# Performance work log

Hardware: AMD Instinct MI355X
Metric: run time of the kernel (lower is better)

Reference implementation:

```python
import jax, jax.numpy as jnp
import numpy as np

DIM = 2048
N_HEAD = 16
HEAD_DIM = DIM // N_HEAD


def setup_inputs() -> dict:
    key = jax.random.key(0)
    ks = jax.random.split(key, 7)
    B, N = 2, 2048
    s = 1.0 / np.sqrt(DIM)
    return {
        "x": jax.random.normal(ks[0], (B, N, DIM), dtype=jnp.float32),
        "Wq": jax.random.normal(ks[1], (DIM, DIM), dtype=jnp.float32) * s,
        "bq": jnp.zeros((DIM,), dtype=jnp.float32),
        "Wkv": jax.random.normal(ks[2], (DIM, 2 * HEAD_DIM), dtype=jnp.float32) * s,
        "bkv": jnp.zeros((2 * HEAD_DIM,), dtype=jnp.float32),
        "Wo": jax.random.normal(ks[3], (DIM, DIM), dtype=jnp.float32) * s,
        "bo": jnp.zeros((DIM,), dtype=jnp.float32),
    }


def reference(x, Wq, bq, Wkv, bkv, Wo, bo):
    B, N, D = x.shape
    # Q projection -> (B, H, N, hd)
    q = (x @ Wq + bq).reshape(B, N, N_HEAD, HEAD_DIM).transpose(0, 2, 1, 3)
    # shared single-head K/V (kv = x, self-attention path)
    kvp = x @ Wkv + bkv  # (B, M, 2*hd)
    k, v = kvp[..., :HEAD_DIM], kvp[..., HEAD_DIM:]  # (B, M, hd) each
    scale = 1.0 / np.sqrt(HEAD_DIM).astype(np.float32)
    # broadcast shared K over heads without materializing expanded K/V
    scores = jnp.einsum("bhnd,bmd->bhnm", q, k) * scale  # (B, H, N, M)
    attn = jax.nn.softmax(scores, axis=-1)
    out = jnp.einsum("bhnm,bmd->bhnd", attn, v)  # (B, H, N, hd)
    out = out.transpose(0, 2, 1, 3).reshape(B, N, D)
    return out @ Wo + bo
```

## Files before the change

kernel.cpp:

```cpp
#include <hip/hip_runtime.h>
#include <math.h>

using bf16x8 = __attribute__((ext_vector_type(8))) short;
using f32x4  = __attribute__((ext_vector_type(4))) float;
using f32x16 = __attribute__((ext_vector_type(16))) float;
using u16x4  = __attribute__((ext_vector_type(4))) unsigned short;
using u32x4  = __attribute__((ext_vector_type(4))) unsigned int;

#define DIMSZ 2048
#define NSEQ  2048
#define BATCH 2
#define NHEAD 16
#define HD    128

__device__ __forceinline__ unsigned short f2bf(float x) {
    unsigned int u = __builtin_bit_cast(unsigned int, x);
    unsigned int r = (u + 0x7FFFu + ((u >> 16) & 1u)) >> 16;
    return (unsigned short)r;
}

__device__ __forceinline__ unsigned int cvtpk_bf16(float lo, float hi) {
    unsigned int r;
    asm("v_cvt_pk_bf16_f32 %0, %1, %2" : "=v"(r) : "v"(lo), "v"(hi));
    return r;
}

__device__ __forceinline__ void gload_lds16(const unsigned short* g, unsigned short* l) {
    __builtin_amdgcn_global_load_lds(
        (const __attribute__((address_space(1))) unsigned int*)g,
        (__attribute__((address_space(3))) unsigned int*)l, 16, 0, 0);
}

__global__ void k_cast_bf16(const float* __restrict__ in, unsigned short* __restrict__ out, int n4) {
    int i = blockIdx.x * blockDim.x + threadIdx.x;
    if (i >= n4) return;
    f32x4 v = *(const f32x4*)(in + (size_t)i * 4);
    u16x4 o;
#pragma unroll
    for (int j = 0; j < 4; j++) o[j] = f2bf(v[j]);
    *(u16x4*)(out + (size_t)i * 4) = o;
}

__global__ void k_transpose_all(const float* __restrict__ Wq, const float* __restrict__ Wkv,
                                const float* __restrict__ Wo, unsigned short* __restrict__ wqkvt,
                                unsigned short* __restrict__ wot, float sc) {
    __shared__ float t[32][33];
    const int ct = blockIdx.x;
    const int k0 = blockIdx.y * 32;
    const float* src;
    unsigned short* dst;
    float scale;
    int N, n0;
    if (ct < 64)      { src = Wq;  dst = wqkvt;                       scale = sc;   N = 2048; n0 = ct * 32; }
    else if (ct < 72) { src = Wkv; dst = wqkvt + (size_t)2048 * 2048; scale = 1.0f; N = 256;  n0 = (ct - 64) * 32; }
    else              { src = Wo;  dst = wot;                         scale = 1.0f; N = 2048; n0 = (ct - 72) * 32; }
    const int tx = threadIdx.x, ty = threadIdx.y;
#pragma unroll
    for (int i = 0; i < 32; i += 8) t[ty + i][tx] = src[(size_t)(k0 + ty + i) * N + n0 + tx];
    __syncthreads();
#pragma unroll
    for (int i = 0; i < 32; i += 8)
        dst[(size_t)(n0 + ty + i) * 2048 + k0 + tx] = f2bf(t[tx][ty + i] * scale);
}

__global__ void k_transpose_v(const unsigned short* __restrict__ kvp, unsigned short* __restrict__ vt) {
    __shared__ unsigned short t[32][33];
    int n0 = blockIdx.x * 32, d0 = blockIdx.y * 32, b = blockIdx.z;
    int tx = threadIdx.x, ty = threadIdx.y;
#pragma unroll
    for (int i = 0; i < 32; i += 8)
        t[ty + i][tx] = kvp[(size_t)(b * NSEQ + n0 + ty + i) * 256 + 128 + d0 + tx];
    __syncthreads();
#pragma unroll
    for (int i = 0; i < 32; i += 8)
        vt[(size_t)(b * HD + d0 + ty + i) * NSEQ + n0 + tx] = t[tx][ty + i];
}

__device__ __forceinline__ void xcd_tile(int nbx, int& bx, int& by) {
    int wg = ((int)blockIdx.x & 7) * ((int)gridDim.x >> 3) + ((int)blockIdx.x >> 3);
    bx = wg % nbx;
    by = wg / nbx;
}

#define GEMM_BODY(EPILOGUE)                                                                    \
    __shared__ unsigned short As[3][256 * 32];                                                 \
    __shared__ unsigned short Bs[3][128 * 32];                                                 \
    const int tid = threadIdx.x;                                                               \
    const int wid = tid >> 6;                                                                  \
    const int lane = tid & 63;                                                                 \
    const int g = lane >> 4, cc = lane & 15;                                                   \
    const int wm = wid >> 1, wn = wid & 1;                                                     \
    int bx, by;                                                                                \
    xcd_tile(nbx, bx, by);                                                                     \
    const size_t m0 = (size_t)by * 256;                                                        \
    const size_t n0 = (size_t)bx * 128;                                                        \
    f32x4 acc[4][4] = {};                                                                      \
               \
    const unsigned short* gA0 = A + (m0 + (tid >> 2)) * (size_t)K + (tid & 3) * 8;             \
    const unsigned short* gA1 = A + (m0 + 128 + (tid >> 2)) * (size_t)K + (tid & 3) * 8;       \
    const unsigned short* gB  = Bt + (n0 + (tid >> 2)) * (size_t)K + (tid & 3) * 8;            \
    const int NT = K / 32;                                                                     \
    auto STAGE = [&](int buf, int k0) {                                                        \
        gload_lds16(gA0 + k0, &As[buf][wid * 512]);                                            \
        gload_lds16(gA1 + k0, &As[buf][4096 + wid * 512]);                                     \
        gload_lds16(gB + k0, &Bs[buf][wid * 512]);                                             \
    };                                                                                         \
    STAGE(0, 0);                                                                               \
    STAGE(1, 32);                                                                              \
    for (int t = 0; t < NT; ++t) {                                                             \
        if (t < NT - 1)                                                                        \
            asm volatile("s_waitcnt vmcnt(3)" ::: "memory");                                   \
        else                                                                                   \
            asm volatile("s_waitcnt vmcnt(0)" ::: "memory");                                   \
        __builtin_amdgcn_s_barrier();                                                          \
        __builtin_amdgcn_sched_barrier(0);                                                     \
        if (t + 2 < NT) STAGE((t + 2) % 3, (t + 2) * 32);                                      \
        const unsigned short* Ac = &As[t % 3][0];                                              \
        const unsigned short* Bc = &Bs[t % 3][0];                                              \
        bf16x8 af[4], bfr[4];                                                                  \
        _Pragma("unroll") for (int mi = 0; mi < 4; mi++)                                       \
            af[mi] = *(const bf16x8*)(Ac + (wm * 64 + mi * 16 + cc) * 32 + g * 8);             \
        _Pragma("unroll") for (int ni = 0; ni < 4; ni++)                                       \
            bfr[ni] = *(const bf16x8*)(Bc + (wn * 64 + ni * 16 + cc) * 32 + g * 8);            \
        _Pragma("unroll") for (int mi = 0; mi < 4; mi++)                                       \
            _Pragma("unroll") for (int ni = 0; ni < 4; ni++)                                   \
                acc[mi][ni] = __builtin_amdgcn_mfma_f32_16x16x32_bf16(af[mi], bfr[ni],         \
                                                                      acc[mi][ni], 0, 0, 0);  \
    }                                                                                          \
    EPILOGUE

__global__ __launch_bounds__(512, 4)
void k_gemm_qkv(const unsigned short* __restrict__ A, const unsigned short* __restrict__ Bt,
                const float* __restrict__ bq, float bscale, const float* __restrict__ bkv,
                unsigned short* __restrict__ qout, unsigned short* __restrict__ kvout,
                int M, int K, int nbx) {
    GEMM_BODY({
        const bool isQ = (n0 < 2048);
        const int colg = (int)n0 + wn * 64 + cc;
        const int col0 = isQ ? colg : colg - 2048;
        const int ostride = isQ ? 2048 : 256;
        unsigned short* outp = isQ ? qout : kvout;
        float bia[4];
        _Pragma("unroll") for (int ni = 0; ni < 4; ni++)
            bia[ni] = isQ ? bq[col0 + ni * 16] * bscale : bkv[col0 + ni * 16];
        _Pragma("unroll") for (int mi = 0; mi < 4; mi++) {
            size_t row = m0 + wm * 64 + mi * 16 + g * 4;
            _Pragma("unroll") for (int ni = 0; ni < 4; ni++)
                _Pragma("unroll") for (int r = 0; r < 4; r++)
                    outp[(row + r) * ostride + col0 + ni * 16] = f2bf(acc[mi][ni][r] + bia[ni]);
        }
    })
}

__global__ __launch_bounds__(512, 4)
void k_gemm_bt_f32(const unsigned short* __restrict__ A, const unsigned short* __restrict__ Bt,
                   const float* __restrict__ bias, float* __restrict__ Cout,
                   int M, int N, int K, int nbx) {
    GEMM_BODY({
        const int col0 = (int)n0 + wn * 64 + cc;
        float bia[4];
        _Pragma("unroll") for (int ni = 0; ni < 4; ni++) bia[ni] = bias[col0 + ni * 16];
        _Pragma("unroll") for (int mi = 0; mi < 4; mi++) {
            size_t row = m0 + wm * 64 + mi * 16 + g * 4;
            _Pragma("unroll") for (int ni = 0; ni < 4; ni++)
                _Pragma("unroll") for (int r = 0; r < 4; r++)
                    Cout[(row + r) * N + col0 + ni * 16] = acc[mi][ni][r] + bia[ni];
        }
    })
}

__global__ __launch_bounds__(256, 2)
void k_attn(const unsigned short* __restrict__ q, const unsigned short* __restrict__ kvp,
            const unsigned short* __restrict__ vt, unsigned short* __restrict__ out) {
    __shared__ unsigned char Kb[2][16384];
    __shared__ unsigned char Vb[2][16384];

    const int b = blockIdx.z, h = blockIdx.y, qt = blockIdx.x;
    const int tid = threadIdx.x, w = tid >> 6, lane = tid & 63;
    const int q32 = lane & 31, hi = lane >> 5;

    const int qrow = qt * 128 + w * 32 + q32;
    const unsigned short* qp = q + (size_t)(b * NSEQ + qrow) * DIMSZ + h * HD + hi * 8;
    bf16x8 qf[8];
#pragma unroll
    for (int dc = 0; dc < 8; dc++) qf[dc] = *(const bf16x8*)(qp + dc * 16);

    const char* kvpc = (const char*)kvp;
    const char* vtc  = (const char*)vt;
    size_t srcK[4], srcV[4];
#pragma unroll
    for (int c = 0; c < 4; c++) {
        unsigned int o = (tid + c * 256) * 16;
        unsigned int krow = o >> 8, kcol = o & 255;
        srcK[c] = (size_t)(b * NSEQ + krow) * 512 + (kcol ^ (((krow >> 1) & 15) << 4));
        unsigned int vrow = o >> 7, vcol = o & 127;
        srcV[c] = (size_t)(b * HD + vrow) * 4096 + (vcol ^ (((vrow >> 2) & 7) << 4));
    }

    auto STAGE = [&](int buf, int t) {
        size_t kb_ = (size_t)t * 32768;
        size_t vb_ = (size_t)t * 128;
#pragma unroll
        for (int c = 0; c < 4; c++) {
            gload_lds16((const unsigned short*)(kvpc + srcK[c] + kb_),
                        (unsigned short*)(Kb[buf] + (w * 64 + c * 256) * 16));
            gload_lds16((const unsigned short*)(vtc + srcV[c] + vb_),
                        (unsigned short*)(Vb[buf] + (w * 64 + c * 256) * 16));
        }
    };

    f32x16 o0 = {}, o1 = {}, o2 = {}, o3 = {};
    float l_run = 0.0f;
    const unsigned int swK = ((q32 >> 1) & 15) << 4;
    const unsigned int swV = ((q32 >> 2) & 7) << 4;

#define PROC_KT(S, KTB)                                                               \
    {                                                                                 \
        float pz[16];                                                                 \
        _Pragma("unroll") for (int r = 0; r < 16; r++) {                              \
            pz[r] = __builtin_amdgcn_exp2f(S[r]);                                     \
            l_run += pz[r];                                                           \
        }                                                                             \
        _Pragma("unroll") for (int kc = 0; kc < 2; kc++) {                            \
            unsigned int own01 = cvtpk_bf16(pz[kc * 8 + 0], pz[kc * 8 + 1]);          \
            unsigned int own23 = cvtpk_bf16(pz[kc * 8 + 2], pz[kc * 8 + 3]);          \
            unsigned int own45 = cvtpk_bf16(pz[kc * 8 + 4], pz[kc * 8 + 5]);          \
            unsigned int own67 = cvtpk_bf16(pz[kc * 8 + 6], pz[kc * 8 + 7]);          \
            unsigned int send_a = hi ? own01 : own45;                                 \
            unsigned int send_b = hi ? own23 : own67;                                 \
            unsigned int got_a = (unsigned int)__shfl_xor((int)send_a, 32, 64);       \
            unsigned int got_b = (unsigned int)__shfl_xor((int)send_b, 32, 64);       \
            u32x4 awv;                                                                \
            awv[0] = hi ? got_a : own01;                                              \
            awv[1] = hi ? got_b : own23;                                              \
            awv[2] = hi ? own45 : got_a;                                              \
            awv[3] = hi ? own67 : got_b;                                              \
            bf16x8 pa = __builtin_bit_cast(bf16x8, awv);                              \
            const unsigned int kbo = (KTB) + kc * 32 + hi * 16;                       \
            bf16x8 vf0 = *(const bf16x8*)(Vc + (q32 + 0) * 128 + (kbo ^ swV));        \
            bf16x8 vf1 = *(const bf16x8*)(Vc + (q32 + 32) * 128 + (kbo ^ swV));       \
            bf16x8 vf2 = *(const bf16x8*)(Vc + (q32 + 64) * 128 + (kbo ^ swV));       \
            bf16x8 vf3 = *(const bf16x8*)(Vc + (q32 + 96) * 128 + (kbo ^ swV));       \
            __builtin_amdgcn_s_setprio(1);                                            \
            o0 = __builtin_amdgcn_mfma_f32_32x32x16_bf16(pa, vf0, o0, 0, 0, 0);       \
            o1 = __builtin_amdgcn_mfma_f32_32x32x16_bf16(pa, vf1, o1, 0, 0, 0);       \
            o2 = __builtin_amdgcn_mfma_f32_32x32x16_bf16(pa, vf2, o2, 0, 0, 0);       \
            o3 = __builtin_amdgcn_mfma_f32_32x32x16_bf16(pa, vf3, o3, 0, 0, 0);       \
            __builtin_amdgcn_s_setprio(0);                                            \
        }                                                                             \
    }

    STAGE(0, 0);
    __syncthreads();

    for (int t = 0; t < NSEQ / 64; t++) {
        const int cur = t & 1;
        if (t < NSEQ / 64 - 1) STAGE(cur ^ 1, t + 1);

        const unsigned char* Kc = Kb[cur];
        const unsigned char* Vc = Vb[cur];

        f32x16 s0 = {}, s1 = {};
#pragma unroll
        for (int dc = 0; dc < 8; dc++) {
            const unsigned int db = dc * 32 + hi * 16;
            bf16x8 kf0 = *(const bf16x8*)(Kc + q32 * 256 + (db ^ swK));
            bf16x8 kf1 = *(const bf16x8*)(Kc + (q32 + 32) * 256 + (db ^ swK));
            __builtin_amdgcn_s_setprio(1);
            s0 = __builtin_amdgcn_mfma_f32_32x32x16_bf16(kf0, qf[dc], s0, 0, 0, 0);
            s1 = __builtin_amdgcn_mfma_f32_32x32x16_bf16(kf1, qf[dc], s1, 0, 0, 0);
            __builtin_amdgcn_s_setprio(0);
        }

        PROC_KT(s0, 0)
        PROC_KT(s1, 64)

        __syncthreads();
    }
#undef PROC_KT

    l_run += __shfl_xor(l_run, 32, 64);
    float* Lp = (float*)(Kb[0] + w * 128);
    if (hi == 0) Lp[q32] = l_run;

    float rinv[16];
#pragma unroll
    for (int r = 0; r < 16; r++) {
        int qloc = (r & 3) + 8 * (r >> 2) + 4 * hi;
        rinv[r] = 1.0f / Lp[qloc];
    }

    unsigned short* op = out + (size_t)(b * NSEQ + qt * 128 + w * 32) * DIMSZ + h * HD + q32;
#pragma unroll
    for (int r = 0; r < 16; r++) {
        int qloc = (r & 3) + 8 * (r >> 2) + 4 * hi;
        op[(size_t)qloc * DIMSZ + 0]  = f2bf(o0[r] * rinv[r]);
        op[(size_t)qloc * DIMSZ + 32] = f2bf(o1[r] * rinv[r]);
        op[(size_t)qloc * DIMSZ + 64] = f2bf(o2[r] * rinv[r]);
        op[(size_t)qloc * DIMSZ + 96] = f2bf(o3[r] * rinv[r]);
    }
}

extern "C" void kernel_launch(void* const* d_in, const int* in_sizes, int n_in,
                              void* d_out, int out_size, void* d_ws, size_t ws_size,
                              hipStream_t stream) {
    const float* x   = (const float*)d_in[0];
    const float* Wq  = (const float*)d_in[1];
    const float* bq  = (const float*)d_in[2];
    const float* Wkv = (const float*)d_in[3];
    const float* bkv = (const float*)d_in[4];
    const float* Wo  = (const float*)d_in[5];
    const float* bo  = (const float*)d_in[6];

    char* w = (char*)d_ws;
    unsigned short* xb    = (unsigned short*)(w);
    unsigned short* wqkvt = (unsigned short*)(w + 16777216);
    unsigned short* wot   = (unsigned short*)(w + 26214400);
    unsigned short* qb    = (unsigned short*)(w + 34603008);
    unsigned short* kvpb  = (unsigned short*)(w + 51380224);
    unsigned short* vtb   = (unsigned short*)(w + 53477376);
    unsigned short* aob   = xb;

    const float sc = 0.08838834764831845f * 1.4426950408889634f;

    k_cast_bf16<<<dim3((BATCH * NSEQ * DIMSZ / 4 + 255) / 256), dim3(256), 0, stream>>>(
        x, xb, BATCH * NSEQ * DIMSZ / 4);
    k_transpose_all<<<dim3(136, 64), dim3(32, 8), 0, stream>>>(Wq, Wkv, Wo, wqkvt, wot, sc);

    k_gemm_qkv<<<dim3((BATCH * NSEQ / 256) * (2304 / 128)), dim3(512), 0, stream>>>(
        xb, wqkvt, bq, sc, bkv, qb, kvpb, BATCH * NSEQ, DIMSZ, 2304 / 128);
    k_transpose_v<<<dim3(NSEQ / 32, HD / 32, BATCH), dim3(32, 8), 0, stream>>>(kvpb, vtb);
    k_attn<<<dim3(NSEQ / 128, NHEAD, BATCH), dim3(256), 0, stream>>>(qb, kvpb, vtb, aob);
    k_gemm_bt_f32<<<dim3((BATCH * NSEQ / 256) * (DIMSZ / 128)), dim3(512), 0, stream>>>(
        aob, wot, bo, (float*)d_out, BATCH * NSEQ, DIMSZ, DIMSZ, DIMSZ / 128);
}
```

Baseline: 224.1 us.

## Merge prep kernels, fuse V transpose into QKV GEMM, retile GEMMs

Folds the x cast and weight transpose into one launch and writes V transposed straight from the QKV GEMM epilogue, which removes two kernel launches and a separate transpose pass. The GEMMs change from 256x128 tiles with 512 threads, K-step 32 and triple buffering to 128x128 tiles with 256 threads, K-step 64 and double buffering with __syncthreads. The new GEMM gives up the fine-grained vmcnt pipelining, so loads and compute may overlap less, and the smaller tiles reuse each loaded tile less.

```diff
diff --git a/kernel.cpp b/kernel.cpp
--- a/kernel.cpp
+++ b/kernel.cpp
@@ -31,22 +31,25 @@
         (__attribute__((address_space(3))) unsigned int*)l, 16, 0, 0);
 }
 
-__global__ void k_cast_bf16(const float* __restrict__ in, unsigned short* __restrict__ out, int n4) {
-    int i = blockIdx.x * blockDim.x + threadIdx.x;
-    if (i >= n4) return;
-    f32x4 v = *(const f32x4*)(in + (size_t)i * 4);
-    u16x4 o;
-#pragma unroll
-    for (int j = 0; j < 4; j++) o[j] = f2bf(v[j]);
-    *(u16x4*)(out + (size_t)i * 4) = o;
-}
-
-__global__ void k_transpose_all(const float* __restrict__ Wq, const float* __restrict__ Wkv,
-                                const float* __restrict__ Wo, unsigned short* __restrict__ wqkvt,
-                                unsigned short* __restrict__ wot, float sc) {
+#define NCAST 8192
+__global__ void k_prep(const float* __restrict__ x, unsigned short* __restrict__ xb,
+                       const float* __restrict__ Wq, const float* __restrict__ Wkv,
+                       const float* __restrict__ Wo, unsigned short* __restrict__ wqkvt,
+                       unsigned short* __restrict__ wot, float sc) {
     __shared__ float t[32][33];
-    const int ct = blockIdx.x;
-    const int k0 = blockIdx.y * 32;
+    const int tid = threadIdx.x;
+    if ((int)blockIdx.x < NCAST) {
+        int i = blockIdx.x * 256 + tid;
+        f32x4 v = *(const f32x4*)(x + (size_t)i * 4);
+        u16x4 o;
+#pragma unroll
+        for (int j = 0; j < 4; j++) o[j] = f2bf(v[j]);
+        *(u16x4*)(xb + (size_t)i * 4) = o;
+        return;
+    }
+    const int tb = blockIdx.x - NCAST;
+    const int ct = tb % 136;
+    const int k0 = (tb / 136) * 32;
     const float* src;
     unsigned short* dst;
     float scale;
@@ -54,26 +57,13 @@
     if (ct < 64)      { src = Wq;  dst = wqkvt;                       scale = sc;   N = 2048; n0 = ct * 32; }
     else if (ct < 72) { src = Wkv; dst = wqkvt + (size_t)2048 * 2048; scale = 1.0f; N = 256;  n0 = (ct - 64) * 32; }
     else              { src = Wo;  dst = wot;                         scale = 1.0f; N = 2048; n0 = (ct - 72) * 32; }
-    const int tx = threadIdx.x, ty = threadIdx.y;
+    const int tx = tid & 31, ty = tid >> 5;
 #pragma unroll
     for (int i = 0; i < 32; i += 8) t[ty + i][tx] = src[(size_t)(k0 + ty + i) * N + n0 + tx];
     __syncthreads();
 #pragma unroll
     for (int i = 0; i < 32; i += 8)
         dst[(size_t)(n0 + ty + i) * 2048 + k0 + tx] = f2bf(t[tx][ty + i] * scale);
-}
-
-__global__ void k_transpose_v(const unsigned short* __restrict__ kvp, unsigned short* __restrict__ vt) {
-    __shared__ unsigned short t[32][33];
-    int n0 = blockIdx.x * 32, d0 = blockIdx.y * 32, b = blockIdx.z;
-    int tx = threadIdx.x, ty = threadIdx.y;
-#pragma unroll
-    for (int i = 0; i < 32; i += 8)
-        t[ty + i][tx] = kvp[(size_t)(b * NSEQ + n0 + ty + i) * 256 + 128 + d0 + tx];
-    __syncthreads();
-#pragma unroll
-    for (int i = 0; i < 32; i += 8)
-        vt[(size_t)(b * HD + d0 + ty + i) * NSEQ + n0 + tx] = t[tx][ty + i];
 }
 
 __device__ __forceinline__ void xcd_tile(int nbx, int& bx, int& by) {
@@ -82,86 +72,103 @@
     by = wg / nbx;
 }
 
-#define GEMM_BODY(EPILOGUE)                                                                    \
-    __shared__ unsigned short As[3][256 * 32];                                                 \
-    __shared__ unsigned short Bs[3][128 * 32];                                                 \
+#define GEMM_BODY64(EPILOGUE)                                                                  \
+    __shared__ unsigned short As[2][128 * 64];                                                 \
+    __shared__ unsigned short Bs[2][128 * 64];                                                 \
     const int tid = threadIdx.x;                                                               \
     const int wid = tid >> 6;                                                                  \
     const int lane = tid & 63;                                                                 \
     const int g = lane >> 4, cc = lane & 15;                                                   \
-    const int wm = wid >> 1, wn = wid & 1;                                                     \
+    const int wr = wid >> 1, wc = wid & 1;                                                     \
     int bx, by;                                                                                \
     xcd_tile(nbx, bx, by);                                                                     \
-    const size_t m0 = (size_t)by * 256;                                                        \
+    const size_t m0 = (size_t)by * 128;                                                        \
     const size_t n0 = (size_t)bx * 128;                                                        \
     f32x4 acc[4][4] = {};                                                                      \
-               \
-    const unsigned short* gA0 = A + (m0 + (tid >> 2)) * (size_t)K + (tid & 3) * 8;             \
-    const unsigned short* gA1 = A + (m0 + 128 + (tid >> 2)) * (size_t)K + (tid & 3) * 8;       \
-    const unsigned short* gB  = Bt + (n0 + (tid >> 2)) * (size_t)K + (tid & 3) * 8;            \
-    const int NT = K / 32;                                                                     \
+    const unsigned short* gA = A + (m0 + wid * 32 + (lane >> 3)) * (size_t)K + (lane & 7) * 8; \
+    const unsigned short* gB = Bt + (n0 + wid * 32 + (lane >> 3)) * (size_t)K + (lane & 7) * 8;\
     auto STAGE = [&](int buf, int k0) {                                                        \
-        gload_lds16(gA0 + k0, &As[buf][wid * 512]);                                            \
-        gload_lds16(gA1 + k0, &As[buf][4096 + wid * 512]);                                     \
-        gload_lds16(gB + k0, &Bs[buf][wid * 512]);                                             \
+        _Pragma("unroll") for (int c = 0; c < 4; c++) {                                        \
+            gload_lds16(gA + (size_t)(c * 8) * K + k0, &As[buf][(wid * 32 + c * 8) * 64]);     \
+            gload_lds16(gB + (size_t)(c * 8) * K + k0, &Bs[buf][(wid * 32 + c * 8) * 64]);     \
+        }                                                                                      \
     };                                                                                         \
     STAGE(0, 0);                                                                               \
-    STAGE(1, 32);                                                                              \
-    for (int t = 0; t < NT; ++t) {                                                             \
-        if (t < NT - 1)                                                                        \
-            asm volatile("s_waitcnt vmcnt(3)" ::: "memory");                                   \
-        else                                                                                   \
-            asm volatile("s_waitcnt vmcnt(0)" ::: "memory");                                   \
-        __builtin_amdgcn_s_barrier();                                                          \
-        __builtin_amdgcn_sched_barrier(0);                                                     \
-        if (t + 2 < NT) STAGE((t + 2) % 3, (t + 2) * 32);                                      \
-        const unsigned short* Ac = &As[t % 3][0];                                              \
-        const unsigned short* Bc = &Bs[t % 3][0];                                              \
-        bf16x8 af[4], bfr[4];                                                                  \
-        _Pragma("unroll") for (int mi = 0; mi < 4; mi++)                                       \
-            af[mi] = *(const bf16x8*)(Ac + (wm * 64 + mi * 16 + cc) * 32 + g * 8);             \
-        _Pragma("unroll") for (int ni = 0; ni < 4; ni++)                                       \
-            bfr[ni] = *(const bf16x8*)(Bc + (wn * 64 + ni * 16 + cc) * 32 + g * 8);            \
-        _Pragma("unroll") for (int mi = 0; mi < 4; mi++)                                       \
+    __syncthreads();                                                                           \
+    int cur = 0;                                                                               \
+    for (int k0 = 0; k0 < K; k0 += 64) {                                                       \
+        if (k0 + 64 < K) STAGE(cur ^ 1, k0 + 64);                                              \
+        _Pragma("unroll") for (int kk = 0; kk < 2; kk++) {                                     \
+            bf16x8 af[4], bfr[4];                                                              \
+            _Pragma("unroll") for (int mi = 0; mi < 4; mi++)                                   \
+                af[mi] = *(const bf16x8*)(&As[cur][(wr * 64 + mi * 16 + cc) * 64 + kk * 32 + g * 8]); \
             _Pragma("unroll") for (int ni = 0; ni < 4; ni++)                                   \
-                acc[mi][ni] = __builtin_amdgcn_mfma_f32_16x16x32_bf16(af[mi], bfr[ni],         \
-                                                                      acc[mi][ni], 0, 0, 0);  \
+                bfr[ni] = *(const bf16x8*)(&Bs[cur][(wc * 64 + ni * 16 + cc) * 64 + kk * 32 + g * 8]); \
+            _Pragma("unroll") for (int mi = 0; mi < 4; mi++)                                   \
+                _Pragma("unroll") for (int ni = 0; ni < 4; ni++)                               \
+                    acc[mi][ni] = __builtin_amdgcn_mfma_f32_16x16x32_bf16(af[mi], bfr[ni],     \
+                                                                          acc[mi][ni], 0, 0, 0); \
+        }                                                                                      \
+        __syncthreads();                                                                       \
+        cur ^= 1;                                                                              \
     }                                                                                          \
     EPILOGUE
 
-__global__ __launch_bounds__(512, 4)
+__global__ __launch_bounds__(256, 2)
 void k_gemm_qkv(const unsigned short* __restrict__ A, const unsigned short* __restrict__ Bt,
                 const float* __restrict__ bq, float bscale, const float* __restrict__ bkv,
                 unsigned short* __restrict__ qout, unsigned short* __restrict__ kvout,
-                int M, int K, int nbx) {
-    GEMM_BODY({
-        const bool isQ = (n0 < 2048);
-        const int colg = (int)n0 + wn * 64 + cc;
-        const int col0 = isQ ? colg : colg - 2048;
-        const int ostride = isQ ? 2048 : 256;
-        unsigned short* outp = isQ ? qout : kvout;
-        float bia[4];
-        _Pragma("unroll") for (int ni = 0; ni < 4; ni++)
-            bia[ni] = isQ ? bq[col0 + ni * 16] * bscale : bkv[col0 + ni * 16];
-        _Pragma("unroll") for (int mi = 0; mi < 4; mi++) {
-            size_t row = m0 + wm * 64 + mi * 16 + g * 4;
-            _Pragma("unroll") for (int ni = 0; ni < 4; ni++)
-                _Pragma("unroll") for (int r = 0; r < 4; r++)
-                    outp[(row + r) * ostride + col0 + ni * 16] = f2bf(acc[mi][ni][r] + bia[ni]);
+                unsigned short* __restrict__ vtout, int M, int K, int nbx) {
+    GEMM_BODY64({
+        if (n0 < 2048) {
+            const int col0 = (int)n0 + wc * 64 + cc;
+            float bia[4];
+            _Pragma("unroll") for (int ni = 0; ni < 4; ni++) bia[ni] = bq[col0 + ni * 16] * bscale;
+            _Pragma("unroll") for (int mi = 0; mi < 4; mi++) {
+                size_t row = m0 + wr * 64 + mi * 16 + g * 4;
+                _Pragma("unroll") for (int ni = 0; ni < 4; ni++)
+                    _Pragma("unroll") for (int r = 0; r < 4; r++)
+                        qout[(row + r) * 2048 + col0 + ni * 16] = f2bf(acc[mi][ni][r] + bia[ni]);
+            }
+        } else if (n0 < 2176) {
+            const int col0 = (int)n0 - 2048 + wc * 64 + cc;
+            float bia[4];
+            _Pragma("unroll") for (int ni = 0; ni < 4; ni++) bia[ni] = bkv[col0 + ni * 16];
+            _Pragma("unroll") for (int mi = 0; mi < 4; mi++) {
+                size_t row = m0 + wr * 64 + mi * 16 + g * 4;
+                _Pragma("unroll") for (int ni = 0; ni < 4; ni++)
+                    _Pragma("unroll") for (int r = 0; r < 4; r++)
+                        kvout[(row + r) * 256 + col0 + ni * 16] = f2bf(acc[mi][ni][r] + bia[ni]);
+            }
+        } else {
+            const int col0 = (int)n0 - 2048 + wc * 64 + cc;
+            float bia[4];
+            _Pragma("unroll") for (int ni = 0; ni < 4; ni++) bia[ni] = bkv[col0 + ni * 16];
+            _Pragma("unroll") for (int mi = 0; mi < 4; mi++) {
+                size_t row = m0 + wr * 64 + mi * 16 + g * 4;
+                const int b = (int)(row >> 11);
+                const int n = (int)(row & 2047);
+                _Pragma("unroll") for (int ni = 0; ni < 4; ni++) {
+                    const int d = col0 + ni * 16 - 128;
+                    u16x4 o;
+                    _Pragma("unroll") for (int r = 0; r < 4; r++) o[r] = f2bf(acc[mi][ni][r] + bia[ni]);
+                    *(u16x4*)(vtout + ((size_t)(b * HD + d)) * NSEQ + n) = o;
+                }
+            }
         }
     })
 }
 
-__global__ __launch_bounds__(512, 4)
+__global__ __launch_bounds__(256, 2)
 void k_gemm_bt_f32(const unsigned short* __restrict__ A, const unsigned short* __restrict__ Bt,
                    const float* __restrict__ bias, float* __restrict__ Cout,
                    int M, int N, int K, int nbx) {
-    GEMM_BODY({
-        const int col0 = (int)n0 + wn * 64 + cc;
+    GEMM_BODY64({
+        const int col0 = (int)n0 + wc * 64 + cc;
         float bia[4];
         _Pragma("unroll") for (int ni = 0; ni < 4; ni++) bia[ni] = bias[col0 + ni * 16];
         _Pragma("unroll") for (int mi = 0; mi < 4; mi++) {
-            size_t row = m0 + wm * 64 + mi * 16 + g * 4;
+            size_t row = m0 + wr * 64 + mi * 16 + g * 4;
             _Pragma("unroll") for (int ni = 0; ni < 4; ni++)
                 _Pragma("unroll") for (int r = 0; r < 4; r++)
                     Cout[(row + r) * N + col0 + ni * 16] = acc[mi][ni][r] + bia[ni];
@@ -323,14 +330,11 @@
 
     const float sc = 0.08838834764831845f * 1.4426950408889634f;
 
-    k_cast_bf16<<<dim3((BATCH * NSEQ * DIMSZ / 4 + 255) / 256), dim3(256), 0, stream>>>(
-        x, xb, BATCH * NSEQ * DIMSZ / 4);
-    k_transpose_all<<<dim3(136, 64), dim3(32, 8), 0, stream>>>(Wq, Wkv, Wo, wqkvt, wot, sc);
-
-    k_gemm_qkv<<<dim3((BATCH * NSEQ / 256) * (2304 / 128)), dim3(512), 0, stream>>>(
-        xb, wqkvt, bq, sc, bkv, qb, kvpb, BATCH * NSEQ, DIMSZ, 2304 / 128);
-    k_transpose_v<<<dim3(NSEQ / 32, HD / 32, BATCH), dim3(32, 8), 0, stream>>>(kvpb, vtb);
+    k_prep<<<dim3(NCAST + 136 * 64), dim3(256), 0, stream>>>(x, xb, Wq, Wkv, Wo, wqkvt, wot, sc);
+
+    k_gemm_qkv<<<dim3((2304 / 128) * (BATCH * NSEQ / 128)), dim3(256), 0, stream>>>(
+        xb, wqkvt, bq, sc, bkv, qb, kvpb, vtb, BATCH * NSEQ, DIMSZ, 2304 / 128);
     k_attn<<<dim3(NSEQ / 128, NHEAD, BATCH), dim3(256), 0, stream>>>(qb, kvpb, vtb, aob);
-    k_gemm_bt_f32<<<dim3((BATCH * NSEQ / 256) * (DIMSZ / 128)), dim3(512), 0, stream>>>(
+    k_gemm_bt_f32<<<dim3((DIMSZ / 128) * (BATCH * NSEQ / 128)), dim3(256), 0, stream>>>(
         aob, wot, bo, (float*)d_out, BATCH * NSEQ, DIMSZ, DIMSZ, DIMSZ / 128);
 }
```

After: 233.3 us. 4.1% more time.
